# Optimization experiments

Measured on AMD Instinct MI355X. Metric: run time of the kernel, lower is better.

## Reference

```python
import jax, jax.numpy as jnp
import numpy as np

# ---- physics constraint targets (constants, precomputed with numpy) ----
_ARC = np.array([[-1,-1,-1],[2,2,2],[-1,-1,-1]], np.float32)
_CURV5 = np.array([[0,0,-1,0,0],[0,-1,2,-1,0],[-1,2,4,2,-1],[0,-1,2,-1,0],[0,0,-1,0,0]], np.float32)
_RAD = np.array([[0,-1,0],[-1,4,-1],[0,-1,0]], np.float32)
_TAN = np.array([[-1,0,-1],[0,4,0],[-1,0,-1]], np.float32)

def _bilinear_1d(a, out_n):
    # torch F.interpolate bilinear, align_corners=False, along axis 0
    n = a.shape[0]
    src = (np.arange(out_n) + 0.5) * n / out_n - 0.5
    i0 = np.clip(np.floor(src).astype(int), 0, n - 1)
    i1 = np.clip(i0 + 1, 0, n - 1)
    f = np.clip(src - np.floor(src), 0.0, 1.0).astype(np.float32)
    shp = (out_n,) + (1,) * (a.ndim - 1)
    return a[i0] * (1 - f).reshape(shp) + a[i1] * f.reshape(shp)

_CURV3 = _bilinear_1d(_bilinear_1d(_CURV5, 3).T, 3).T  # 5x5 -> 3x3 separable bilinear
CONSTRAINTS = jnp.asarray(np.stack([_ARC, _CURV3, _RAD, _TAN]))  # [4,3,3]

NUM_HEADS = 4
PHYSICS_WEIGHT = 0.1


def setup_inputs() -> dict:
    key = jax.random.key(0)
    ks = jax.random.split(key, 6)
    B, N, C = 8, 1024, 256
    return {
        "x": jax.random.normal(ks[0], (B, N, C), jnp.float32),
        "qkv_w": jax.random.normal(ks[1], (3 * C, C), jnp.float32) * (C ** -0.5),
        "qkv_b": jax.random.normal(ks[2], (3 * C,), jnp.float32) * 0.02,
        "proj_w": jax.random.normal(ks[3], (C, C), jnp.float32) * (C ** -0.5),
        "proj_b": jax.random.normal(ks[4], (C,), jnp.float32) * 0.02,
        "kernels": jax.random.normal(ks[5], (4, 3, 3), jnp.float32) * 0.1,
        "H": 32,
        "W": 32,
    }


def _physics_prior(x, kernels, H, W):
    # Original: depthwise conv each channel with each kernel, mean over kernels,
    # mean over channels, sigmoid, outer product. Conv + means are linear, so
    # mean-over-kernels and mean-over-channels commute with the (shared-kernel)
    # depthwise conv: conv(mean_C(x), mean_k(kernels)).
    B, N, C = x.shape
    xm = x.mean(axis=2).reshape(B, 1, H, W)            # [B,1,H,W]
    kmean = kernels.mean(axis=0)[None, None]           # [1,1,3,3] (OIHW)
    conv = jax.lax.conv_general_dilated(
        xm, kmean, window_strides=(1, 1), padding=((1, 1), (1, 1)),
        dimension_numbers=("NCHW", "OIHW", "NCHW"))
    amap = jax.nn.sigmoid(conv.reshape(B, N))          # [B,N]
    return amap[:, :, None] * amap[:, None, :]         # [B,N,N]


def _reg_loss(kernels):
    mse = jnp.mean((kernels - CONSTRAINTS) ** 2, axis=(1, 2)).sum()
    l1 = 0.01 * jnp.abs(kernels).sum()
    return mse + l1


def reference(x, qkv_w, qkv_b, proj_w, proj_b, kernels, H, W):
    B, N, C = x.shape
    hd = C // NUM_HEADS
    scale = hd ** -0.5
    qkv = (x @ qkv_w.T + qkv_b).reshape(B, N, 3, NUM_HEADS, hd)
    qkv = qkv.transpose(2, 0, 3, 1, 4)                 # [3,B,h,N,hd]
    q, k, v = qkv[0], qkv[1], qkv[2]
    attn = jnp.einsum("bhnd,bhmd->bhnm", q, k) * scale  # [B,h,N,N]
    prior = _physics_prior(x, kernels, H, W)            # [B,N,N]
    attn = attn + PHYSICS_WEIGHT * prior[:, None]
    attn = jax.nn.softmax(attn, axis=-1)                # dropout: eval mode (identity)
    out = jnp.einsum("bhnm,bhmd->bhnd", attn, v)
    out = out.transpose(0, 2, 1, 3).reshape(B, N, C)
    out = out @ proj_w.T + proj_b
    attention_weights = attn.mean(axis=1)               # [B,N,N]
    return out, attention_weights, _reg_loss(kernels)
```

## Files before the change

### kernel.cpp

```cpp
#include <hip/hip_runtime.h>
#include <cstdint>

typedef _Float16 h16;
typedef __attribute__((ext_vector_type(8))) _Float16 f16x8;
typedef __attribute__((ext_vector_type(4))) _Float16 f16x4;
typedef __attribute__((ext_vector_type(4))) float f32x4;

#define L2E 1.44269504f

__global__ void k_cast(const float* __restrict__ x, const float* __restrict__ qw,
                       const float* __restrict__ pw, h16* __restrict__ xh,
                       h16* __restrict__ qwh, h16* __restrict__ pwh,
                       float* __restrict__ xm) {
  int bid = blockIdx.x, tid = threadIdx.x;
  if (bid < 2048) {
    int i4 = bid * 256 + tid;
    float4 v = ((const float4*)x)[i4];
    f16x4 o = {(h16)v.x, (h16)v.y, (h16)v.z, (h16)v.w};
    ((f16x4*)xh)[i4] = o;
    float s = v.x + v.y + v.z + v.w;
#pragma unroll
    for (int off = 32; off; off >>= 1) s += __shfl_xor(s, off);
    if ((tid & 63) == 0) xm[i4 >> 6] = s * (1.0f / 256.0f);
  } else {
    int i4 = (bid - 2048) * 256 + tid;
    if (i4 < 49152) {
      float4 v = ((const float4*)qw)[i4];
      f16x4 o = {(h16)v.x, (h16)v.y, (h16)v.z, (h16)v.w};
      ((f16x4*)qwh)[i4] = o;
    } else {
      int j = i4 - 49152;
      float4 v = ((const float4*)pw)[j];
      f16x4 o = {(h16)v.x, (h16)v.y, (h16)v.z, (h16)v.w};
      ((f16x4*)pwh)[j] = o;
    }
  }
}

__global__ void k_amap(const float* __restrict__ xm,
                       const float* __restrict__ kern,
                       float* __restrict__ amap) {
  int idx = blockIdx.x * 256 + threadIdx.x;
  int b = idx >> 10, n = idx & 1023;
  int y = n >> 5, xq = n & 31;
  float km[9];
#pragma unroll
  for (int i = 0; i < 9; ++i)
    km[i] = 0.25f * (kern[i] + kern[9 + i] + kern[18 + i] + kern[27 + i]);
  float acc = 0.f;
#pragma unroll
  for (int dy = 0; dy < 3; ++dy) {
#pragma unroll
    for (int dx = 0; dx < 3; ++dx) {
      int yy = y + dy - 1, xx = xq + dx - 1;
      if (yy >= 0 && yy < 32 && xx >= 0 && xx < 32)
        acc += km[dy * 3 + dx] * xm[(b << 10) + (yy << 5) + xx];
    }
  }
  amap[idx] = 1.0f / (1.0f + __expf(-acc));
}

__global__ __launch_bounds__(128) void k_qkv(
    const h16* __restrict__ xh, const h16* __restrict__ qwh,
    const float* __restrict__ bias, h16* __restrict__ Qh,
    h16* __restrict__ Kh, h16* __restrict__ Vt) {
  const int w = threadIdx.x >> 6, lane = threadIdx.x & 63;
  const int g = lane >> 4, li = lane & 15;
  const int tile = blockIdx.x * 2 + w;
  const int tr = tile & 255, tc = tile >> 8;
  const int r0 = tr * 32, c0 = tc * 64;
  f32x4 acc[2][4];
#pragma unroll
  for (int mr = 0; mr < 2; ++mr)
#pragma unroll
    for (int nc = 0; nc < 4; ++nc) acc[mr][nc] = {0.f, 0.f, 0.f, 0.f};
  for (int ks = 0; ks < 8; ++ks) {
    int k0 = ks * 32 + g * 8;
    f16x8 a[2], bf[4];
#pragma unroll
    for (int mr = 0; mr < 2; ++mr)
      a[mr] = *(const f16x8*)(xh + (size_t)(r0 + mr * 16 + li) * 256 + k0);
#pragma unroll
    for (int nc = 0; nc < 4; ++nc)
      bf[nc] = *(const f16x8*)(qwh + (size_t)(c0 + nc * 16 + li) * 256 + k0);
#pragma unroll
    for (int mr = 0; mr < 2; ++mr)
#pragma unroll
      for (int nc = 0; nc < 4; ++nc)
        acc[mr][nc] = __builtin_amdgcn_mfma_f32_16x16x32_f16(a[mr], bf[nc],
                                                             acc[mr][nc], 0, 0, 0);
  }
  const int which = c0 >> 8;
  const int hh = (c0 >> 6) & 3;
#pragma unroll
  for (int nc = 0; nc < 4; ++nc) {
    int d = nc * 16 + li;
    float bv = bias[c0 + d];
#pragma unroll
    for (int mr = 0; mr < 2; ++mr) {
#pragma unroll
      for (int r = 0; r < 4; ++r) {
        int m = r0 + mr * 16 + g * 4 + r;
        int bq = m >> 10, n = m & 1023;
        float v = acc[mr][nc][r] + bv;
        size_t base = ((size_t)(bq * 4 + hh)) << 16;
        if (which == 0) Qh[base + (size_t)n * 64 + d] = (h16)v;
        else if (which == 1) Kh[base + (size_t)n * 64 + d] = (h16)v;
        else Vt[base + (size_t)d * 1024 + n] = (h16)v;
      }
    }
  }
}

__global__ void k_knorm(const h16* __restrict__ Kh, float* __restrict__ Kmaxb) {
  __shared__ float red[4];
  const int tid = threadIdx.x;
  const h16* base = Kh + ((size_t)blockIdx.x << 16);
  float mx = 0.f;
#pragma unroll
  for (int i = 0; i < 4; ++i) {
    int n = i * 256 + tid;
    float s2 = 0.f;
#pragma unroll
    for (int ks = 0; ks < 8; ++ks) {
      f16x8 v = *(const f16x8*)(base + (size_t)n * 64 + ks * 8);
#pragma unroll
      for (int e = 0; e < 8; ++e) {
        float f = (float)v[e];
        s2 += f * f;
      }
    }
    mx = fmaxf(mx, s2);
  }
#pragma unroll
  for (int off = 32; off; off >>= 1) mx = fmaxf(mx, __shfl_xor(mx, off));
  if ((tid & 63) == 0) red[tid >> 6] = mx;
  __syncthreads();
  if (tid == 0) {
    mx = fmaxf(fmaxf(red[0], red[1]), fmaxf(red[2], red[3]));
    Kmaxb[blockIdx.x] = sqrtf(mx);
  }
}

__global__ __launch_bounds__(512, 4) void k_attn(
    const h16* __restrict__ Qh, const h16* __restrict__ Kh,
    const h16* __restrict__ Vt, const float* __restrict__ amap,
    const float* __restrict__ Kmaxb, h16* __restrict__ Pg,
    float* __restrict__ rinvb, h16* __restrict__ OHh) {
  __shared__ float am_s[1024];
  __shared__ float Lsh[4][2][16];
  __shared__ float Osh[4][16][64];
  __shared__ __align__(16) unsigned char Pst[8][2048];

  const int tid = threadIdx.x;
  const int wave = tid >> 6, lane = tid & 63, g = lane >> 4, li = lane & 15;
  const int h = wave >> 1, jh = wave & 1;
  const int b = blockIdx.x & 7, rt = blockIdx.x >> 3;
  const int r0 = rt * 16;
  const int bh = b * 4 + h;
  const size_t base = ((size_t)bh) << 16;

  am_s[tid] = amap[(b << 10) + tid];
  am_s[tid + 512] = amap[(b << 10) + 512 + tid];
  __syncthreads();

  f16x8 qf[2];
#pragma unroll
  for (int ks = 0; ks < 2; ++ks)
    qf[ks] = *(const f16x8*)(Qh + base + (size_t)(r0 + li) * 64 + ks * 32 + g * 8);

  float nq2 = 0.f;
#pragma unroll
  for (int ks = 0; ks < 2; ++ks)
#pragma unroll
    for (int e = 0; e < 8; ++e) {
      float f = (float)qf[ks][e];
      nq2 += f * f;
    }
  nq2 += __shfl_xor(nq2, 16);
  nq2 += __shfl_xor(nq2, 32);
  float c_li = 0.125f * sqrtf(nq2) * Kmaxb[bh] + 0.11f;
  float cr2[4], amr2[4];
#pragma unroll
  for (int r = 0; r < 4; ++r) {
    cr2[r] = __shfl(c_li, g * 4 + r) * L2E;
    amr2[r] = 0.1f * L2E * am_s[r0 + g * 4 + r];
  }

  float lpart[4] = {0.f, 0.f, 0.f, 0.f};
  f32x4 o[4];
#pragma unroll
  for (int nd = 0; nd < 4; ++nd) o[nd] = {0.f, 0.f, 0.f, 0.f};

  for (int jj = 0; jj < 8; ++jj) {
    const int j0 = (jh * 8 + jj) << 6;
    f16x8 kf[4][2];
#pragma unroll
    for (int nc = 0; nc < 4; ++nc)
#pragma unroll
      for (int ks = 0; ks < 2; ++ks)
        kf[nc][ks] = *(const f16x8*)(Kh + base + (size_t)(j0 + nc * 16 + li) * 64 +
                                     ks * 32 + g * 8);
    f32x4 s[4];
#pragma unroll
    for (int nc = 0; nc < 4; ++nc) {
      f32x4 a = {0.f, 0.f, 0.f, 0.f};
      a = __builtin_amdgcn_mfma_f32_16x16x32_f16(qf[0], kf[nc][0], a, 0, 0, 0);
      a = __builtin_amdgcn_mfma_f32_16x16x32_f16(qf[1], kf[nc][1], a, 0, 0, 0);
      s[nc] = a;
    }
#pragma unroll
    for (int nc = 0; nc < 4; ++nc) {
      float amc = am_s[j0 + nc * 16 + li];
      int colb = (nc * 16 + li) * 2;
#pragma unroll
      for (int r = 0; r < 4; ++r) {
        float p = exp2f(s[nc][r] * (0.125f * L2E) + amr2[r] * amc - cr2[r]);
        lpart[r] += p;
        int row = g * 4 + r;
        *(h16*)(&Pst[wave][(row << 7) + (colb ^ ((row & 7) << 4))]) = (h16)p;
      }
    }
    f16x8 af[2];
#pragma unroll
    for (int ks = 0; ks < 2; ++ks) {
      int cb = (ks * 32 + g * 8) * 2;
      af[ks] = *(const f16x8*)(&Pst[wave][(li << 7) + (cb ^ ((li & 7) << 4))]);
      *(f16x8*)(Pg + ((size_t)bh << 20) + (size_t)(r0 + li) * 1024 + j0 +
                ks * 32 + g * 8) = af[ks];
    }
#pragma unroll
    for (int nd = 0; nd < 4; ++nd) {
      f16x8 v0 = *(const f16x8*)(Vt + base + (size_t)(nd * 16 + li) * 1024 + j0 +
                                 g * 8);
      f16x8 v1 = *(const f16x8*)(Vt + base + (size_t)(nd * 16 + li) * 1024 + j0 +
                                 32 + g * 8);
      o[nd] = __builtin_amdgcn_mfma_f32_16x16x32_f16(af[0], v0, o[nd], 0, 0, 0);
      o[nd] = __builtin_amdgcn_mfma_f32_16x16x32_f16(af[1], v1, o[nd], 0, 0, 0);
    }
  }

#pragma unroll
  for (int r = 0; r < 4; ++r) {
    lpart[r] += __shfl_xor(lpart[r], 1);
    lpart[r] += __shfl_xor(lpart[r], 2);
    lpart[r] += __shfl_xor(lpart[r], 4);
    lpart[r] += __shfl_xor(lpart[r], 8);
  }
  if (li == 0) {
#pragma unroll
    for (int r = 0; r < 4; ++r) Lsh[h][jh][g * 4 + r] = lpart[r];
  }
  __syncthreads();
  float rinv[4];
#pragma unroll
  for (int r = 0; r < 4; ++r)
    rinv[r] = 1.0f / (Lsh[h][0][g * 4 + r] + Lsh[h][1][g * 4 + r]);
  if (jh == 1) {
#pragma unroll
    for (int nd = 0; nd < 4; ++nd)
#pragma unroll
      for (int r = 0; r < 4; ++r) Osh[h][g * 4 + r][nd * 16 + li] = o[nd][r];
  }
  __syncthreads();
  if (jh == 0) {
#pragma unroll
    for (int nd = 0; nd < 4; ++nd)
#pragma unroll
      for (int r = 0; r < 4; ++r) {
        float v = (o[nd][r] + Osh[h][g * 4 + r][nd * 16 + li]) * rinv[r];
        OHh[(size_t)((b << 10) + r0 + g * 4 + r) * 256 + h * 64 + nd * 16 + li] =
            (h16)v;
      }
    if (li == 0) {
#pragma unroll
      for (int r = 0; r < 4; ++r)
        rinvb[((size_t)bh << 10) + r0 + g * 4 + r] = rinv[r];
    }
  }
}

__global__ void k_awnorm(const h16* __restrict__ Pg,
                         const float* __restrict__ rinvb,
                         float* __restrict__ AW) {
  int idx = blockIdx.x * 256 + threadIdx.x;
  int b = idx >> 17;
  int rem = idx & 131071;
  int i = rem >> 7;
  int jc = (rem & 127) << 3;
  size_t rowbase = ((size_t)i << 10) + jc;
  float sum[8] = {0.f, 0.f, 0.f, 0.f, 0.f, 0.f, 0.f, 0.f};
#pragma unroll
  for (int h = 0; h < 4; ++h) {
    int bh = b * 4 + h;
    f16x8 pu = *(const f16x8*)(Pg + (((size_t)bh) << 20) + rowbase);
    float rv = 0.25f * rinvb[((size_t)bh << 10) + i];
#pragma unroll
    for (int e = 0; e < 8; ++e) sum[e] += (float)pu[e] * rv;
  }
  float* dst = AW + (((size_t)b) << 20) + rowbase;
  float4 o1 = {sum[0], sum[1], sum[2], sum[3]};
  float4 o2 = {sum[4], sum[5], sum[6], sum[7]};
  *(float4*)dst = o1;
  *(float4*)(dst + 4) = o2;
}

__global__ __launch_bounds__(128) void k_proj(const h16* __restrict__ OHh,
                                              const h16* __restrict__ pwh,
                                              const float* __restrict__ bias,
                                              float* __restrict__ out) {
  const int w = threadIdx.x >> 6, lane = threadIdx.x & 63;
  const int g = lane >> 4, li = lane & 15;
  const int tile = blockIdx.x * 2 + w;
  const int tc = tile & 3, tr = tile >> 2;
  const int r0 = tr * 32, c0 = tc * 64;
  f32x4 acc[2][4];
#pragma unroll
  for (int mr = 0; mr < 2; ++mr)
#pragma unroll
    for (int nc = 0; nc < 4; ++nc) acc[mr][nc] = {0.f, 0.f, 0.f, 0.f};
  for (int ks = 0; ks < 8; ++ks) {
    int k0 = ks * 32 + g * 8;
    f16x8 a[2], bf[4];
#pragma unroll
    for (int mr = 0; mr < 2; ++mr)
      a[mr] = *(const f16x8*)(OHh + (size_t)(r0 + mr * 16 + li) * 256 + k0);
#pragma unroll
    for (int nc = 0; nc < 4; ++nc)
      bf[nc] = *(const f16x8*)(pwh + (size_t)(c0 + nc * 16 + li) * 256 + k0);
#pragma unroll
    for (int mr = 0; mr < 2; ++mr)
#pragma unroll
      for (int nc = 0; nc < 4; ++nc)
        acc[mr][nc] = __builtin_amdgcn_mfma_f32_16x16x32_f16(a[mr], bf[nc],
                                                             acc[mr][nc], 0, 0, 0);
  }
#pragma unroll
  for (int nc = 0; nc < 4; ++nc) {
    int c = c0 + nc * 16 + li;
    float bv = bias[c];
#pragma unroll
    for (int mr = 0; mr < 2; ++mr)
#pragma unroll
      for (int r = 0; r < 4; ++r) {
        int m = r0 + mr * 16 + g * 4 + r;
        out[(size_t)m * 256 + c] = acc[mr][nc][r] + bv;
      }
  }
}

__global__ void k_reg(const float* __restrict__ kern, float* __restrict__ out) {
  const float Cst[36] = {
      -1.f, -1.f, -1.f, 2.f, 2.f, 2.f, -1.f, -1.f, -1.f,
      -0.11111111f, 0.f, -0.11111111f, 0.f, 4.f, 0.f,
      -0.11111111f, 0.f, -0.11111111f,
      0.f, -1.f, 0.f, -1.f, 4.f, -1.f, 0.f, -1.f, 0.f,
      -1.f, 0.f, -1.f, 0.f, 4.f, 0.f, -1.f, 0.f, -1.f};
  int t = threadIdx.x;
  float v = 0.f;
  if (t < 36) {
    float kv = kern[t];
    float d = kv - Cst[t];
    v = d * d * (1.0f / 9.0f) + 0.01f * fabsf(kv);
  }
#pragma unroll
  for (int off = 32; off; off >>= 1) v += __shfl_xor(v, off);
  if (t == 0) out[0] = v;
}

extern "C" void kernel_launch(void* const* d_in, const int* in_sizes, int n_in,
                              void* d_out, int out_size, void* d_ws,
                              size_t ws_size, hipStream_t stream) {
  const float* x = (const float*)d_in[0];
  const float* qkv_w = (const float*)d_in[1];
  const float* qkv_b = (const float*)d_in[2];
  const float* proj_w = (const float*)d_in[3];
  const float* proj_b = (const float*)d_in[4];
  const float* kern = (const float*)d_in[5];

  float* out = (float*)d_out;
  float* aw = out + 2097152;
  float* rl = out + 10485760;

  float* xm = (float*)d_ws;
  float* amap = xm + 8192;
  float* rinvb = amap + 8192;
  float* Kmaxb = rinvb + 32768;
  h16* xh = (h16*)(Kmaxb + 64);
  h16* qwh = xh + 2097152;
  h16* pwh = qwh + 196608;
  h16* Qh = pwh + 65536;
  h16* Kh = Qh + 2097152;
  h16* Vt = Kh + 2097152;
  h16* OHh = Vt + 2097152;
  h16* Pg = OHh + 2097152;

  k_cast<<<2304, 256, 0, stream>>>(x, qkv_w, proj_w, xh, qwh, pwh, xm);
  k_amap<<<32, 256, 0, stream>>>(xm, kern, amap);
  k_qkv<<<1536, 128, 0, stream>>>(xh, qwh, qkv_b, Qh, Kh, Vt);
  k_knorm<<<32, 256, 0, stream>>>(Kh, Kmaxb);
  k_attn<<<512, 512, 0, stream>>>(Qh, Kh, Vt, amap, Kmaxb, Pg, rinvb, OHh);
  k_awnorm<<<4096, 256, 0, stream>>>(Pg, rinvb, aw);
  k_proj<<<512, 128, 0, stream>>>(OHh, pwh, proj_b, out);
  k_reg<<<1, 64, 0, stream>>>(kern, rl);
}
```

Measured before the change: 222.2 us.

## Precompute row log-sum-exp in separate pass and fuse head-averaged weights into attention

Adds a k_lsum pass that computes each row's normalizer (as a log2 offset) ahead of time. The attention kernel can then emit normalized probabilities directly and average them across the four heads in shared memory before writing the fp32 attention-weight matrix. This drops the fp16 probability buffer Pg and the separate k_awnorm pass, along with their large global write and read. In exchange the QK^T products and exponentials are computed twice, and each 64-column step of the attention loop now has two block-wide barriers. It also vectorizes the V-transpose stores in the QKV epilogue and transposes the MFMA operand order so each lane holds contiguous outputs.

```diff
diff --git a/kernel.cpp b/kernel.cpp
--- a/kernel.cpp
+++ b/kernel.cpp
@@ -7,6 +7,7 @@
 typedef __attribute__((ext_vector_type(4))) float f32x4;
 
 #define L2E 1.44269504f
+#define QSCALE (0.125f * L2E)
 
 __global__ void k_cast(const float* __restrict__ x, const float* __restrict__ qw,
                        const float* __restrict__ pw, h16* __restrict__ xh,
@@ -92,21 +93,34 @@
   }
   const int which = c0 >> 8;
   const int hh = (c0 >> 6) & 3;
-#pragma unroll
-  for (int nc = 0; nc < 4; ++nc) {
-    int d = nc * 16 + li;
-    float bv = bias[c0 + d];
-#pragma unroll
-    for (int mr = 0; mr < 2; ++mr) {
-#pragma unroll
-      for (int r = 0; r < 4; ++r) {
-        int m = r0 + mr * 16 + g * 4 + r;
-        int bq = m >> 10, n = m & 1023;
-        float v = acc[mr][nc][r] + bv;
-        size_t base = ((size_t)(bq * 4 + hh)) << 16;
-        if (which == 0) Qh[base + (size_t)n * 64 + d] = (h16)v;
-        else if (which == 1) Kh[base + (size_t)n * 64 + d] = (h16)v;
-        else Vt[base + (size_t)d * 1024 + n] = (h16)v;
+  const int bq = r0 >> 10;
+  const size_t base = ((size_t)(bq * 4 + hh)) << 16;
+  if (which == 2) {
+#pragma unroll
+    for (int nc = 0; nc < 4; ++nc) {
+      int d = nc * 16 + li;
+      float bv = bias[c0 + d];
+#pragma unroll
+      for (int mr = 0; mr < 2; ++mr) {
+        int n0 = (r0 & 1023) + mr * 16 + g * 4;
+        f16x4 pk = {(h16)(acc[mr][nc][0] + bv), (h16)(acc[mr][nc][1] + bv),
+                    (h16)(acc[mr][nc][2] + bv), (h16)(acc[mr][nc][3] + bv)};
+        *(f16x4*)(Vt + base + (size_t)d * 1024 + n0) = pk;
+      }
+    }
+  } else {
+    h16* dst = (which == 0) ? Qh : Kh;
+#pragma unroll
+    for (int nc = 0; nc < 4; ++nc) {
+      int d = nc * 16 + li;
+      float bv = bias[c0 + d];
+#pragma unroll
+      for (int mr = 0; mr < 2; ++mr) {
+#pragma unroll
+        for (int r = 0; r < 4; ++r) {
+          int n = (r0 & 1023) + mr * 16 + g * 4 + r;
+          dst[base + (size_t)n * 64 + d] = (h16)(acc[mr][nc][r] + bv);
+        }
       }
     }
   }
@@ -142,15 +156,86 @@
   }
 }
 
+__global__ __launch_bounds__(256, 4) void k_lsum(
+    const h16* __restrict__ Qh, const h16* __restrict__ Kh,
+    const float* __restrict__ amap, const float* __restrict__ Kmaxb,
+    float* __restrict__ Erow) {
+  __shared__ float am_s[1024];
+  __shared__ float Lsh[2][2][16];
+  const int tid = threadIdx.x;
+  const int wave = tid >> 6, lane = tid & 63, g = lane >> 4, li = lane & 15;
+  const int qsub = wave >> 1, jh = wave & 1;
+  const int bh = blockIdx.x >> 5, rt = blockIdx.x & 31;
+  const int b = bh >> 2;
+  const int r0 = rt * 32 + qsub * 16;
+  const size_t base = ((size_t)bh) << 16;
+
+  am_s[tid] = amap[(b << 10) + tid];
+  am_s[tid + 256] = amap[(b << 10) + 256 + tid];
+  am_s[tid + 512] = amap[(b << 10) + 512 + tid];
+  am_s[tid + 768] = amap[(b << 10) + 768 + tid];
+  __syncthreads();
+
+  f16x8 qf[2];
+#pragma unroll
+  for (int ks = 0; ks < 2; ++ks)
+    qf[ks] = *(const f16x8*)(Qh + base + (size_t)(r0 + li) * 64 + ks * 32 + g * 8);
+
+  float nq2 = 0.f;
+#pragma unroll
+  for (int ks = 0; ks < 2; ++ks)
+#pragma unroll
+    for (int e = 0; e < 8; ++e) {
+      float f = (float)qf[ks][e];
+      nq2 += f * f;
+    }
+  nq2 += __shfl_xor(nq2, 16);
+  nq2 += __shfl_xor(nq2, 32);
+  const float c = 0.125f * sqrtf(nq2) * Kmaxb[bh] + 0.11f;
+  const float mcl = -c * L2E;
+  const float amr2 = 0.1f * L2E * am_s[r0 + li];
+  const int prow = ((li >> 2) << 3) + (li & 3);
+
+  float lpart = 0.f;
+  for (int jj = 0; jj < 8; ++jj) {
+    const int j0 = jh * 512 + jj * 64;
+#pragma unroll
+    for (int u = 0; u < 2; ++u) {
+#pragma unroll
+      for (int ab = 0; ab < 2; ++ab) {
+        const int rK = j0 + u * 32 + ab * 4 + prow;
+        f16x8 k0 = *(const f16x8*)(Kh + base + (size_t)rK * 64 + g * 8);
+        f16x8 k1 = *(const f16x8*)(Kh + base + (size_t)rK * 64 + 32 + g * 8);
+        f32x4 s = {0.f, 0.f, 0.f, 0.f};
+        s = __builtin_amdgcn_mfma_f32_16x16x32_f16(k0, qf[0], s, 0, 0, 0);
+        s = __builtin_amdgcn_mfma_f32_16x16x32_f16(k1, qf[1], s, 0, 0, 0);
+        f32x4 am4 = *(const f32x4*)&am_s[j0 + u * 32 + g * 8 + ab * 4];
+#pragma unroll
+        for (int r = 0; r < 4; ++r) {
+          float pre = fmaf(amr2, am4[r], mcl);
+          lpart += exp2f(fmaf(s[r], QSCALE, pre));
+        }
+      }
+    }
+  }
+  lpart += __shfl_xor(lpart, 16);
+  lpart += __shfl_xor(lpart, 32);
+  if (g == 0) Lsh[qsub][jh][li] = lpart;
+  __syncthreads();
+  if (jh == 0 && g == 0) {
+    float l = Lsh[qsub][0][li] + Lsh[qsub][1][li];
+    Erow[((size_t)bh << 10) + r0 + li] = c * L2E + __log2f(l);
+  }
+}
+
 __global__ __launch_bounds__(512, 4) void k_attn(
     const h16* __restrict__ Qh, const h16* __restrict__ Kh,
     const h16* __restrict__ Vt, const float* __restrict__ amap,
-    const float* __restrict__ Kmaxb, h16* __restrict__ Pg,
-    float* __restrict__ rinvb, h16* __restrict__ OHh) {
+    const float* __restrict__ Erow, float* __restrict__ AW,
+    h16* __restrict__ OHh) {
   __shared__ float am_s[1024];
-  __shared__ float Lsh[4][2][16];
-  __shared__ float Osh[4][16][64];
   __shared__ __align__(16) unsigned char Pst[8][2048];
+  __shared__ float Osh[4][16][68];
 
   const int tid = threadIdx.x;
   const int wave = tid >> 6, lane = tid & 63, g = lane >> 4, li = lane & 15;
@@ -169,140 +254,84 @@
   for (int ks = 0; ks < 2; ++ks)
     qf[ks] = *(const f16x8*)(Qh + base + (size_t)(r0 + li) * 64 + ks * 32 + g * 8);
 
-  float nq2 = 0.f;
-#pragma unroll
-  for (int ks = 0; ks < 2; ++ks)
-#pragma unroll
-    for (int e = 0; e < 8; ++e) {
-      float f = (float)qf[ks][e];
-      nq2 += f * f;
-    }
-  nq2 += __shfl_xor(nq2, 16);
-  nq2 += __shfl_xor(nq2, 32);
-  float c_li = 0.125f * sqrtf(nq2) * Kmaxb[bh] + 0.11f;
-  float cr2[4], amr2[4];
-#pragma unroll
-  for (int r = 0; r < 4; ++r) {
-    cr2[r] = __shfl(c_li, g * 4 + r) * L2E;
-    amr2[r] = 0.1f * L2E * am_s[r0 + g * 4 + r];
-  }
-
-  float lpart[4] = {0.f, 0.f, 0.f, 0.f};
+  const float E = Erow[((size_t)bh << 10) + r0 + li];
+  const float amr2 = 0.1f * L2E * am_s[r0 + li];
+  const int prow = ((li >> 2) << 3) + (li & 3);
+  const int swz = (li & 7) << 4;
+
   f32x4 o[4];
 #pragma unroll
   for (int nd = 0; nd < 4; ++nd) o[nd] = {0.f, 0.f, 0.f, 0.f};
 
+  const int arow = tid >> 5, ac = (tid & 31) << 2;
+  const int ahalf = ac >> 6, aci = ac & 63;
+  const int aswz = (arow & 7) << 4;
+
   for (int jj = 0; jj < 8; ++jj) {
-    const int j0 = (jh * 8 + jj) << 6;
-    f16x8 kf[4][2];
-#pragma unroll
-    for (int nc = 0; nc < 4; ++nc)
-#pragma unroll
-      for (int ks = 0; ks < 2; ++ks)
-        kf[nc][ks] = *(const f16x8*)(Kh + base + (size_t)(j0 + nc * 16 + li) * 64 +
-                                     ks * 32 + g * 8);
-    f32x4 s[4];
-#pragma unroll
-    for (int nc = 0; nc < 4; ++nc) {
-      f32x4 a = {0.f, 0.f, 0.f, 0.f};
-      a = __builtin_amdgcn_mfma_f32_16x16x32_f16(qf[0], kf[nc][0], a, 0, 0, 0);
-      a = __builtin_amdgcn_mfma_f32_16x16x32_f16(qf[1], kf[nc][1], a, 0, 0, 0);
-      s[nc] = a;
-    }
-#pragma unroll
-    for (int nc = 0; nc < 4; ++nc) {
-      float amc = am_s[j0 + nc * 16 + li];
-      int colb = (nc * 16 + li) * 2;
-#pragma unroll
-      for (int r = 0; r < 4; ++r) {
-        float p = exp2f(s[nc][r] * (0.125f * L2E) + amr2[r] * amc - cr2[r]);
-        lpart[r] += p;
-        int row = g * 4 + r;
-        *(h16*)(&Pst[wave][(row << 7) + (colb ^ ((row & 7) << 4))]) = (h16)p;
-      }
-    }
-    f16x8 af[2];
-#pragma unroll
-    for (int ks = 0; ks < 2; ++ks) {
-      int cb = (ks * 32 + g * 8) * 2;
-      af[ks] = *(const f16x8*)(&Pst[wave][(li << 7) + (cb ^ ((li & 7) << 4))]);
-      *(f16x8*)(Pg + ((size_t)bh << 20) + (size_t)(r0 + li) * 1024 + j0 +
-                ks * 32 + g * 8) = af[ks];
+    const int j0 = jh * 512 + jj * 64;
+    f16x8 bfrag[2];
+#pragma unroll
+    for (int u = 0; u < 2; ++u) {
+      f32x4 s[2];
+      f32x4 am4[2];
+#pragma unroll
+      for (int ab = 0; ab < 2; ++ab) {
+        const int rK = j0 + u * 32 + ab * 4 + prow;
+        f16x8 k0 = *(const f16x8*)(Kh + base + (size_t)rK * 64 + g * 8);
+        f16x8 k1 = *(const f16x8*)(Kh + base + (size_t)rK * 64 + 32 + g * 8);
+        f32x4 a = {0.f, 0.f, 0.f, 0.f};
+        a = __builtin_amdgcn_mfma_f32_16x16x32_f16(k0, qf[0], a, 0, 0, 0);
+        a = __builtin_amdgcn_mfma_f32_16x16x32_f16(k1, qf[1], a, 0, 0, 0);
+        s[ab] = a;
+        am4[ab] = *(const f32x4*)&am_s[j0 + u * 32 + g * 8 + ab * 4];
+      }
+      f16x8 bf;
+#pragma unroll
+      for (int ab = 0; ab < 2; ++ab)
+#pragma unroll
+        for (int r = 0; r < 4; ++r) {
+          float pre = fmaf(amr2, am4[ab][r], -E);
+          bf[ab * 4 + r] = (h16)exp2f(fmaf(s[ab][r], QSCALE, pre));
+        }
+      bfrag[u] = bf;
+      *(f16x8*)(&Pst[wave][(li << 7) + ((u * 64 + g * 16) ^ swz)]) = bf;
     }
 #pragma unroll
     for (int nd = 0; nd < 4; ++nd) {
-      f16x8 v0 = *(const f16x8*)(Vt + base + (size_t)(nd * 16 + li) * 1024 + j0 +
-                                 g * 8);
-      f16x8 v1 = *(const f16x8*)(Vt + base + (size_t)(nd * 16 + li) * 1024 + j0 +
-                                 32 + g * 8);
-      o[nd] = __builtin_amdgcn_mfma_f32_16x16x32_f16(af[0], v0, o[nd], 0, 0, 0);
-      o[nd] = __builtin_amdgcn_mfma_f32_16x16x32_f16(af[1], v1, o[nd], 0, 0, 0);
-    }
-  }
-
-#pragma unroll
-  for (int r = 0; r < 4; ++r) {
-    lpart[r] += __shfl_xor(lpart[r], 1);
-    lpart[r] += __shfl_xor(lpart[r], 2);
-    lpart[r] += __shfl_xor(lpart[r], 4);
-    lpart[r] += __shfl_xor(lpart[r], 8);
-  }
-  if (li == 0) {
-#pragma unroll
-    for (int r = 0; r < 4; ++r) Lsh[h][jh][g * 4 + r] = lpart[r];
-  }
-  __syncthreads();
-  float rinv[4];
-#pragma unroll
-  for (int r = 0; r < 4; ++r)
-    rinv[r] = 1.0f / (Lsh[h][0][g * 4 + r] + Lsh[h][1][g * 4 + r]);
+      f16x8 v0 = *(const f16x8*)(Vt + base + (size_t)(nd * 16 + li) * 1024 + j0 + g * 8);
+      f16x8 v1 = *(const f16x8*)(Vt + base + (size_t)(nd * 16 + li) * 1024 + j0 + 32 + g * 8);
+      o[nd] = __builtin_amdgcn_mfma_f32_16x16x32_f16(v0, bfrag[0], o[nd], 0, 0, 0);
+      o[nd] = __builtin_amdgcn_mfma_f32_16x16x32_f16(v1, bfrag[1], o[nd], 0, 0, 0);
+    }
+    __syncthreads();
+    {
+      float s0 = 0.f, s1 = 0.f, s2 = 0.f, s3 = 0.f;
+#pragma unroll
+      for (int h2 = 0; h2 < 4; ++h2) {
+        f16x4 v = *(const f16x4*)(&Pst[h2 * 2 + ahalf][(arow << 7) + ((aci * 2) ^ aswz)]);
+        s0 += (float)v[0]; s1 += (float)v[1]; s2 += (float)v[2]; s3 += (float)v[3];
+      }
+      const int colg = ahalf * 512 + jj * 64 + aci;
+      float4 ov = {0.25f * s0, 0.25f * s1, 0.25f * s2, 0.25f * s3};
+      *(float4*)(AW + ((size_t)b << 20) + (size_t)(r0 + arow) * 1024 + colg) = ov;
+    }
+    __syncthreads();
+  }
   if (jh == 1) {
 #pragma unroll
     for (int nd = 0; nd < 4; ++nd)
-#pragma unroll
-      for (int r = 0; r < 4; ++r) Osh[h][g * 4 + r][nd * 16 + li] = o[nd][r];
+      *(f32x4*)&Osh[h][li][nd * 16 + g * 4] = o[nd];
   }
   __syncthreads();
   if (jh == 0) {
 #pragma unroll
-    for (int nd = 0; nd < 4; ++nd)
-#pragma unroll
-      for (int r = 0; r < 4; ++r) {
-        float v = (o[nd][r] + Osh[h][g * 4 + r][nd * 16 + li]) * rinv[r];
-        OHh[(size_t)((b << 10) + r0 + g * 4 + r) * 256 + h * 64 + nd * 16 + li] =
-            (h16)v;
-      }
-    if (li == 0) {
-#pragma unroll
-      for (int r = 0; r < 4; ++r)
-        rinvb[((size_t)bh << 10) + r0 + g * 4 + r] = rinv[r];
-    }
-  }
-}
-
-__global__ void k_awnorm(const h16* __restrict__ Pg,
-                         const float* __restrict__ rinvb,
-                         float* __restrict__ AW) {
-  int idx = blockIdx.x * 256 + threadIdx.x;
-  int b = idx >> 17;
-  int rem = idx & 131071;
-  int i = rem >> 7;
-  int jc = (rem & 127) << 3;
-  size_t rowbase = ((size_t)i << 10) + jc;
-  float sum[8] = {0.f, 0.f, 0.f, 0.f, 0.f, 0.f, 0.f, 0.f};
-#pragma unroll
-  for (int h = 0; h < 4; ++h) {
-    int bh = b * 4 + h;
-    f16x8 pu = *(const f16x8*)(Pg + (((size_t)bh) << 20) + rowbase);
-    float rv = 0.25f * rinvb[((size_t)bh << 10) + i];
-#pragma unroll
-    for (int e = 0; e < 8; ++e) sum[e] += (float)pu[e] * rv;
-  }
-  float* dst = AW + (((size_t)b) << 20) + rowbase;
-  float4 o1 = {sum[0], sum[1], sum[2], sum[3]};
-  float4 o2 = {sum[4], sum[5], sum[6], sum[7]};
-  *(float4*)dst = o1;
-  *(float4*)(dst + 4) = o2;
+    for (int nd = 0; nd < 4; ++nd) {
+      f32x4 p = *(const f32x4*)&Osh[h][li][nd * 16 + g * 4];
+      f16x4 pk = {(h16)(o[nd][0] + p[0]), (h16)(o[nd][1] + p[1]),
+                  (h16)(o[nd][2] + p[2]), (h16)(o[nd][3] + p[3])};
+      *(f16x4*)(OHh + (size_t)((b << 10) + r0 + li) * 256 + h * 64 + nd * 16 + g * 4) = pk;
+    }
+  }
 }
 
 __global__ __launch_bounds__(128) void k_proj(const h16* __restrict__ OHh,
@@ -337,14 +366,14 @@
   }
 #pragma unroll
   for (int nc = 0; nc < 4; ++nc) {
-    int c = c0 + nc * 16 + li;
-    float bv = bias[c];
+    int cc = c0 + nc * 16 + li;
+    float bv = bias[cc];
 #pragma unroll
     for (int mr = 0; mr < 2; ++mr)
 #pragma unroll
       for (int r = 0; r < 4; ++r) {
         int m = r0 + mr * 16 + g * 4 + r;
-        out[(size_t)m * 256 + c] = acc[mr][nc][r] + bv;
+        out[(size_t)m * 256 + cc] = acc[mr][nc][r] + bv;
       }
   }
 }
@@ -384,8 +413,8 @@
 
   float* xm = (float*)d_ws;
   float* amap = xm + 8192;
-  float* rinvb = amap + 8192;
-  float* Kmaxb = rinvb + 32768;
+  float* Erow = amap + 8192;
+  float* Kmaxb = Erow + 32768;
   h16* xh = (h16*)(Kmaxb + 64);
   h16* qwh = xh + 2097152;
   h16* pwh = qwh + 196608;
@@ -393,14 +422,13 @@
   h16* Kh = Qh + 2097152;
   h16* Vt = Kh + 2097152;
   h16* OHh = Vt + 2097152;
-  h16* Pg = OHh + 2097152;
 
   k_cast<<<2304, 256, 0, stream>>>(x, qkv_w, proj_w, xh, qwh, pwh, xm);
   k_amap<<<32, 256, 0, stream>>>(xm, kern, amap);
   k_qkv<<<1536, 128, 0, stream>>>(xh, qwh, qkv_b, Qh, Kh, Vt);
   k_knorm<<<32, 256, 0, stream>>>(Kh, Kmaxb);
-  k_attn<<<512, 512, 0, stream>>>(Qh, Kh, Vt, amap, Kmaxb, Pg, rinvb, OHh);
-  k_awnorm<<<4096, 256, 0, stream>>>(Pg, rinvb, aw);
+  k_lsum<<<1024, 256, 0, stream>>>(Qh, Kh, amap, Kmaxb, Erow);
+  k_attn<<<512, 512, 0, stream>>>(Qh, Kh, Vt, amap, Erow, aw, OHh);
   k_proj<<<512, 128, 0, stream>>>(OHh, pwh, proj_b, out);
   k_reg<<<1, 64, 0, stream>>>(kern, rl);
 }
```

Result: no change. 219.8 us (-1.1%).
